# Optimization experiments

Measured on AMD Instinct MI355X. Metric: run time of the kernel, lower is better.

Reference implementation:

```python
import jax, jax.numpy as jnp
import numpy as np

N_NODES = 50000
N_EDGES = 800000
D_IN = 128
D_HID = 128
N_CLASSES = 10


def gcn_conv(x, edge_index, edge_weight, W, b):
    """PyG GCNConv with edge weights: add self-loops, symmetric deg^-1/2 norm,
    gather-scale-scatter aggregation, then bias."""
    n = x.shape[0]
    row, col = edge_index[0], edge_index[1]
    loop = jnp.arange(n)
    row = jnp.concatenate([row, loop])
    col = jnp.concatenate([col, loop])
    ew = jnp.concatenate([edge_weight, jnp.ones((n,), edge_weight.dtype)])
    # degree computed at target nodes (source_to_target flow)
    deg = jax.ops.segment_sum(ew, col, num_segments=n)
    dinv = jnp.where(deg > 0, jax.lax.rsqrt(deg), 0.0)
    norm = dinv[row] * ew * dinv[col]  # [E+N]
    xw = x @ W  # [N, D_HID] dense GEMM first (PyG order)
    msgs = norm[:, None] * xw[row]  # [E+N, D_HID] edge-wise gather+scale
    out = jax.ops.segment_sum(msgs, col, num_segments=n)  # scatter-add
    return out + b


def setup_inputs() -> dict:
    key = jax.random.key(0)
    ks = jax.random.split(key, 9)
    x = jax.random.normal(ks[0], (N_NODES, D_IN), dtype=jnp.float32)
    edge_index = jax.random.randint(ks[1], (2, N_EDGES), 0, N_NODES, dtype=jnp.int64)
    edge_attr = jax.random.uniform(ks[2], (N_EDGES,), dtype=jnp.float32)
    s1 = 1.0 / np.sqrt(D_IN)
    s2 = 1.0 / np.sqrt(D_HID)
    W1 = jax.random.uniform(ks[3], (D_IN, D_HID), minval=-s1, maxval=s1, dtype=jnp.float32)
    b1 = jnp.zeros((D_HID,), jnp.float32)
    W2 = jax.random.uniform(ks[4], (D_HID, D_HID), minval=-s2, maxval=s2, dtype=jnp.float32)
    b2 = jnp.zeros((D_HID,), jnp.float32)
    Wm = jax.random.uniform(ks[5], (D_HID, N_CLASSES), minval=-s2, maxval=s2, dtype=jnp.float32)
    bm = jax.random.uniform(ks[6], (N_CLASSES,), minval=-s2, maxval=s2, dtype=jnp.float32)
    return {"x": x, "edge_index": edge_index, "edge_attr": edge_attr,
            "W1": W1, "b1": b1, "W2": W2, "b2": b2, "Wm": Wm, "bm": bm}


def reference(x, edge_index, edge_attr, W1, b1, W2, b2, Wm, bm):
    h = jax.nn.relu(gcn_conv(x, edge_index, edge_attr, W1, b1))
    h = jax.nn.relu(gcn_conv(h, edge_index, edge_attr, W2, b2))
    # F.dropout(training=False) is identity in eval mode
    g = jnp.mean(h, axis=0)  # [D_HID] graph readout
    return g @ Wm + bm  # [N_CLASSES]
```

## Files before the change

### kernel.cpp

```cpp
#include <hip/hip_runtime.h>

#define DD 128
#define CAP 8192

typedef __attribute__((ext_vector_type(8))) short short8v;
typedef __attribute__((ext_vector_type(4))) float float4v;

__device__ inline unsigned short f2b(float f) {
    unsigned int x = __float_as_uint(f);
    return (unsigned short)((x + 0x7fffu + ((x >> 16) & 1u)) >> 16);
}
__device__ inline float blo(unsigned int u) { return __uint_as_float(u << 16); }
__device__ inline float bhi(unsigned int u) { return __uint_as_float(u & 0xffff0000u); }

__global__ void wconv2_kernel(const float* __restrict__ W1, unsigned short* __restrict__ Wt1h,
                              unsigned short* __restrict__ Wt1l,
                              const float* __restrict__ W2, unsigned short* __restrict__ Wt2h,
                              unsigned short* __restrict__ Wt2l,
                              int* bcnt, int nb) {
    int t = threadIdx.x;
    if (blockIdx.x == 0 && t < nb) bcnt[t] = 0;
    int which = blockIdx.x >> 6;
    int idx = (blockIdx.x & 63) * 256 + t;
    int k = idx >> 7, nn = idx & 127;
    const float* W = which ? W2 : W1;
    unsigned short* Hh = which ? Wt2h : Wt1h;
    unsigned short* Hl = which ? Wt2l : Wt1l;
    float w = W[idx];
    unsigned short hi = f2b(w);
    float rem = w - __uint_as_float(((unsigned int)hi) << 16);
    Hh[nn * 128 + k] = hi;
    Hl[nn * 128 + k] = f2b(rem);
}

__global__ __launch_bounds__(256) void bin_direct_kernel(const int* __restrict__ row,
                                                         const int* __restrict__ col,
                                                         const float* __restrict__ ew,
                                                         int* bcnt, uint2* __restrict__ binned,
                                                         int E) {
    __shared__ int h[256];
    __shared__ int resv[256];
    int t = threadIdx.x;
    h[t] = 0;
    __syncthreads();
    int base = blockIdx.x * 2048;
    int myb[8], myrank[8];
    uint2 myrec[8];
    bool val[8];
#pragma unroll
    for (int j = 0; j < 8; ++j) {
        int e = base + j * 256 + t;
        val[j] = e < E;
        if (val[j]) {
            int c = col[e], r = row[e];
            myb[j] = c >> 8;
            myrank[j] = atomicAdd(&h[myb[j]], 1);
            myrec[j] = make_uint2(__float_as_uint(ew[e]),
                                  ((unsigned int)r << 8) | (unsigned int)(c & 255));
        }
    }
    __syncthreads();
    if (h[t]) resv[t] = atomicAdd(&bcnt[t], h[t]);
    __syncthreads();
#pragma unroll
    for (int j = 0; j < 8; ++j)
        if (val[j]) {
            int pos = resv[myb[j]] + myrank[j];
            if (pos < CAP) binned[(size_t)myb[j] * CAP + pos] = myrec[j];
        }
}

__global__ __launch_bounds__(256) void build_csr_kernel(const uint2* __restrict__ binned,
                                                        const int* __restrict__ bcnt,
                                                        uint2* __restrict__ startend,
                                                        float* __restrict__ dinv,
                                                        unsigned int* __restrict__ sedge, int n) {
    __shared__ unsigned int cnt[256];
    __shared__ unsigned int degf[256];
    __shared__ int sc[256];
    __shared__ int cur[256];
    int b = blockIdx.x, t = threadIdx.x;
    cnt[t] = 0; degf[t] = 0;
    __syncthreads();
    const int total = bcnt[b];
    const uint2* brec = binned + (size_t)b * CAP;
    for (int k = t; k < total; k += 256) {
        uint2 rec = brec[k];
        int cl = rec.y & 255;
        atomicAdd(&cnt[cl], 1u);
        atomicAdd(&degf[cl], (unsigned int)__float2uint_rn(__uint_as_float(rec.x) * 16777216.0f));
    }
    __syncthreads();
    int v = (int)cnt[t];
    sc[t] = v;
    __syncthreads();
    for (int off = 1; off < 256; off <<= 1) {
        int add = t >= off ? sc[t - off] : 0;
        __syncthreads();
        sc[t] += add;
        __syncthreads();
    }
    const int bstart = b * CAP;
    int myStart = bstart + sc[t] - v;
    cur[t] = myStart;
    int node = b * 256 + t;
    if (node < n) {
        startend[node] = make_uint2((unsigned int)myStart, (unsigned int)(myStart + v));
        float deg = 1.0f + (float)((double)degf[t] * (1.0 / 16777216.0));
        dinv[node] = 1.0f / sqrtf(deg);
    }
    __syncthreads();
    for (int k = t; k < total; k += 256) {
        uint2 rec = brec[k];
        int cl = rec.y & 255;
        int r = (int)(rec.y >> 8);
        int pos = atomicAdd(&cur[cl], 1);
        sedge[pos] = ((unsigned int)r << 16) | (unsigned int)f2b(__uint_as_float(rec.x));
    }
}

template <bool F32A>
__global__ __launch_bounds__(256) void mfma_gemm_kernel(const void* __restrict__ Av,
                                                        const unsigned short* __restrict__ WtHi,
                                                        const unsigned short* __restrict__ WtLo,
                                                        const float* __restrict__ dinv,
                                                        unsigned short* __restrict__ C, int n) {
    __shared__ __align__(16) unsigned short WLh[16 * 128 * 8];
    __shared__ __align__(16) unsigned short WLl[16 * 128 * 8];
    const int tid = threadIdx.x;

    for (int c = tid; c < 2048; c += 256) {
        int nn = c >> 4, k8 = c & 15;
        short8v vh = *(const short8v*)(WtHi + nn * 128 + k8 * 8);
        short8v vl = *(const short8v*)(WtLo + nn * 128 + k8 * 8);
        *(short8v*)(WLh + (k8 * 128 + nn) * 8) = vh;
        *(short8v*)(WLl + (k8 * 128 + nn) * 8) = vl;
    }
    __syncthreads();

    const int lane = tid & 63;
    const int l15 = lane & 15, l4 = lane >> 4;
    const int m0 = blockIdx.x * 128 + (tid >> 6) * 32;

    float4v acc[2][8];
#pragma unroll
    for (int i = 0; i < 2; ++i)
#pragma unroll
        for (int j = 0; j < 8; ++j) acc[i][j] = (float4v){0.f, 0.f, 0.f, 0.f};

#pragma unroll
    for (int kb = 0; kb < 4; ++kb) {
        short8v aF[2];
#pragma unroll
        for (int i = 0; i < 2; ++i) {
            int r = m0 + i * 16 + l15;
            r = r < n ? r : n - 1;
            if constexpr (F32A) {
                const float* xr = (const float*)Av + (size_t)r * 128 + kb * 32 + l4 * 8;
                float4 v0 = ((const float4*)xr)[0];
                float4 v1 = ((const float4*)xr)[1];
                short8v a;
                a[0] = (short)f2b(v0.x); a[1] = (short)f2b(v0.y);
                a[2] = (short)f2b(v0.z); a[3] = (short)f2b(v0.w);
                a[4] = (short)f2b(v1.x); a[5] = (short)f2b(v1.y);
                a[6] = (short)f2b(v1.z); a[7] = (short)f2b(v1.w);
                aF[i] = a;
            } else {
                aF[i] = *(const short8v*)((const unsigned short*)Av +
                                          (size_t)r * 128 + kb * 32 + l4 * 8);
            }
        }
        const int k8 = kb * 4 + l4;
#pragma unroll
        for (int j = 0; j < 8; ++j) {
            short8v bh = *(const short8v*)(WLh + (k8 * 128 + j * 16 + l15) * 8);
            short8v bl = *(const short8v*)(WLl + (k8 * 128 + j * 16 + l15) * 8);
            acc[0][j] = __builtin_amdgcn_mfma_f32_16x16x32_bf16(aF[0], bh, acc[0][j], 0, 0, 0);
            acc[1][j] = __builtin_amdgcn_mfma_f32_16x16x32_bf16(aF[1], bh, acc[1][j], 0, 0, 0);
            acc[0][j] = __builtin_amdgcn_mfma_f32_16x16x32_bf16(aF[0], bl, acc[0][j], 0, 0, 0);
            acc[1][j] = __builtin_amdgcn_mfma_f32_16x16x32_bf16(aF[1], bl, acc[1][j], 0, 0, 0);
        }
    }

#pragma unroll
    for (int i = 0; i < 2; ++i)
#pragma unroll
        for (int r = 0; r < 4; ++r) {
            int rr = m0 + i * 16 + l4 * 4 + r;
            if (rr < n) {
                float dvr = dinv[rr];
#pragma unroll
                for (int j = 0; j < 8; ++j)
                    C[(size_t)rr * 128 + j * 16 + l15] = f2b(acc[i][j][r] * dvr);
            }
        }
}

__device__ inline void agg_node(int i, int t, const uint2* __restrict__ startend,
                                const unsigned int* __restrict__ sedge,
                                const float* __restrict__ dinv,
                                const unsigned short* __restrict__ xw,
                                const float* __restrict__ bias,
                                float& a0out, float& a1out) {
    unsigned int u = *(const unsigned int*)(xw + (size_t)i * DD + 2 * t);
    float a0 = blo(u);
    float a1 = bhi(u);
    uint2 se = startend[i];
    int k = (int)se.x;
    const int e = (int)se.y;
    for (; k + 15 < e; k += 16) {
        unsigned int pe[16], uu[16];
        float nv[16];
#pragma unroll
        for (int j = 0; j < 16; ++j) pe[j] = sedge[k + j];
#pragma unroll
        for (int j = 0; j < 16; ++j) {
            nv[j] = __uint_as_float((pe[j] & 0xffffu) << 16);
            uu[j] = *(const unsigned int*)(xw + (size_t)(pe[j] >> 16) * DD + 2 * t);
        }
#pragma unroll
        for (int j = 0; j < 16; ++j) {
            a0 += nv[j] * blo(uu[j]);
            a1 += nv[j] * bhi(uu[j]);
        }
    }
    for (; k + 3 < e; k += 4) {
        unsigned int pe[4], uu[4];
        float nv[4];
#pragma unroll
        for (int j = 0; j < 4; ++j) pe[j] = sedge[k + j];
#pragma unroll
        for (int j = 0; j < 4; ++j) {
            nv[j] = __uint_as_float((pe[j] & 0xffffu) << 16);
            uu[j] = *(const unsigned int*)(xw + (size_t)(pe[j] >> 16) * DD + 2 * t);
        }
#pragma unroll
        for (int j = 0; j < 4; ++j) {
            a0 += nv[j] * blo(uu[j]);
            a1 += nv[j] * bhi(uu[j]);
        }
    }
    for (; k < e; ++k) {
        unsigned int pe = sedge[k];
        float nvv = __uint_as_float((pe & 0xffffu) << 16);
        unsigned int u2 = *(const unsigned int*)(xw + (size_t)(pe >> 16) * DD + 2 * t);
        a0 += nvv * blo(u2);
        a1 += nvv * bhi(u2);
    }
    const float dv = dinv[i];
    a0out = fmaxf(dv * a0 + bias[2 * t], 0.f);
    a1out = fmaxf(dv * a1 + bias[2 * t + 1], 0.f);
}

__global__ __launch_bounds__(256) void agg_kernel(const uint2* __restrict__ startend,
                                                  const unsigned int* __restrict__ sedge,
                                                  const float* __restrict__ dinv,
                                                  const unsigned short* __restrict__ xw,
                                                  const float* __restrict__ bias,
                                                  unsigned short* __restrict__ h, int n) {
    const int i = blockIdx.x * 4 + (threadIdx.x >> 6);
    if (i >= n) return;
    const int t = threadIdx.x & 63;
    float a0, a1;
    agg_node(i, t, startend, sedge, dinv, xw, bias, a0, a1);
    *(unsigned int*)(h + (size_t)i * DD + 2 * t) =
        (unsigned int)f2b(a0) | ((unsigned int)f2b(a1) << 16);
}

__global__ __launch_bounds__(256) void agg_colsum_kernel(const uint2* __restrict__ startend,
                                                         const unsigned int* __restrict__ sedge,
                                                         const float* __restrict__ dinv,
                                                         const unsigned short* __restrict__ xw,
                                                         const float* __restrict__ bias,
                                                         float* __restrict__ partial, int n) {
    __shared__ float red[4][64][2];
    const int w = threadIdx.x >> 6;
    const int t = threadIdx.x & 63;
    const int i = blockIdx.x * 4 + w;
    float a0 = 0.f, a1 = 0.f;
    if (i < n) agg_node(i, t, startend, sedge, dinv, xw, bias, a0, a1);
    red[w][t][0] = a0;
    red[w][t][1] = a1;
    __syncthreads();
    if (threadIdx.x < DD) {
        int f = threadIdx.x, tt = f >> 1, idx = f & 1;
        float s = red[0][tt][idx] + red[1][tt][idx] + red[2][tt][idx] + red[3][tt][idx];
        partial[(size_t)blockIdx.x * DD + f] = s;
    }
}

__global__ __launch_bounds__(128) void colsum2_kernel(const float* __restrict__ partial,
                                                      float* __restrict__ partial2, int nblk) {
    int t = threadIdx.x;
    float acc = 0.f;
    for (int r = blockIdx.x; r < nblk; r += gridDim.x) acc += partial[(size_t)r * DD + t];
    partial2[blockIdx.x * DD + t] = acc;
}

__global__ void final_kernel(const float* __restrict__ partial2, const float* __restrict__ Wm,
                             const float* __restrict__ bm, float* __restrict__ out, int n) {
    __shared__ float g[DD];
    int t = threadIdx.x;
    float acc = 0.f;
    for (int b = 0; b < 512; ++b) acc += partial2[b * DD + t];
    g[t] = acc / (float)n;
    __syncthreads();
    if (t < 10) {
        float o = bm[t];
#pragma unroll
        for (int d = 0; d < DD; ++d) o += g[d] * Wm[d * 10 + t];
        out[t] = o;
    }
}

extern "C" void kernel_launch(void* const* d_in, const int* in_sizes, int n_in,
                              void* d_out, int out_size, void* d_ws, size_t ws_size,
                              hipStream_t stream) {
    const float* x  = (const float*)d_in[0];
    const int*   ei = (const int*)d_in[1];
    const float* ew = (const float*)d_in[2];
    const float* W1 = (const float*)d_in[3];
    const float* b1 = (const float*)d_in[4];
    const float* W2 = (const float*)d_in[5];
    const float* b2 = (const float*)d_in[6];
    const float* Wm = (const float*)d_in[7];
    const float* bm = (const float*)d_in[8];
    float* out = (float*)d_out;

    const int n = in_sizes[0] / DD;
    const int E = in_sizes[2];
    const int* row = ei;
    const int* col = ei + E;

    const int nb = (n + 255) >> 8;
    const int edgeChunks = (E + 2047) / 2048;
    const int aggBlocks = (n + 3) / 4;

    uint2* binned = (uint2*)d_ws;
    unsigned int* sedge = (unsigned int*)(binned + (size_t)nb * CAP);
    float* dinv    = (float*)(sedge + (size_t)nb * CAP);
    uint2* startend = (uint2*)(dinv + n);
    int*   bcnt    = (int*)(startend + n);
    float* partial = (float*)(bcnt + nb);
    float* partial2 = partial + (size_t)aggBlocks * DD;
    uintptr_t p = (uintptr_t)(partial2 + 512 * DD);
    p = (p + 15) & ~(uintptr_t)15;
    unsigned short* T0 = (unsigned short*)p;
    unsigned short* T1 = T0 + (size_t)n * DD;
    unsigned short* Wt1h = T1 + (size_t)n * DD;
    unsigned short* Wt1l = Wt1h + 16384;
    unsigned short* Wt2h = Wt1l + 16384;
    unsigned short* Wt2l = Wt2h + 16384;

    wconv2_kernel<<<128, 256, 0, stream>>>(W1, Wt1h, Wt1l, W2, Wt2h, Wt2l, bcnt, nb);

    bin_direct_kernel<<<edgeChunks, 256, 0, stream>>>(row, col, ew, bcnt, binned, E);
    build_csr_kernel<<<nb, 256, 0, stream>>>(binned, bcnt, startend, dinv, sedge, n);

    const int gemmBlocks = (n + 127) / 128;

    mfma_gemm_kernel<true><<<gemmBlocks, 256, 0, stream>>>(x, Wt1h, Wt1l, dinv, T0, n);
    agg_kernel<<<aggBlocks, 256, 0, stream>>>(startend, sedge, dinv, T0, b1, T1, n);

    mfma_gemm_kernel<false><<<gemmBlocks, 256, 0, stream>>>(T1, Wt2h, Wt2l, dinv, T0, n);
    agg_colsum_kernel<<<aggBlocks, 256, 0, stream>>>(startend, sedge, dinv, T0, b2, partial, n);

    colsum2_kernel<<<512, 128, 0, stream>>>(partial, partial2, aggBlocks);
    final_kernel<<<1, 128, 0, stream>>>(partial2, Wm, bm, out, n);
}
```

Baseline: 168.1 us.

## Split each node's edges across 4 lane groups with 16-byte row gathers

Rewrites the aggregation so each wavefront splits its node's edge list across four 16-lane groups. Each lane loads 16 bytes (8 bf16 features) per neighbor row instead of 4, and the partial sums are combined with cross-lane xor shuffles. The aim is fewer, wider gather instructions and more neighbor rows in flight per wave, which should raise memory-level parallelism for this bandwidth- and latency-bound gather. The cost is extra shuffle reductions, idle predicated lanes on low-degree nodes, and only a quarter of the lanes doing the final store.

```diff
diff --git a/kernel.cpp b/kernel.cpp
--- a/kernel.cpp
+++ b/kernel.cpp
@@ -196,60 +196,63 @@
         }
 }
 
-__device__ inline void agg_node(int i, int t, const uint2* __restrict__ startend,
-                                const unsigned int* __restrict__ sedge,
-                                const float* __restrict__ dinv,
-                                const unsigned short* __restrict__ xw,
-                                const float* __restrict__ bias,
-                                float& a0out, float& a1out) {
-    unsigned int u = *(const unsigned int*)(xw + (size_t)i * DD + 2 * t);
-    float a0 = blo(u);
-    float a1 = bhi(u);
+__device__ inline void agg_node_v4(int i, int sub, int q,
+                                   const uint2* __restrict__ startend,
+                                   const unsigned int* __restrict__ sedge,
+                                   const float* __restrict__ dinv,
+                                   const unsigned short* __restrict__ xw,
+                                   const float* __restrict__ bias,
+                                   float* __restrict__ a) {
+#pragma unroll
+    for (int j = 0; j < 8; ++j) a[j] = 0.f;
+    const uint4* xw4 = (const uint4*)xw;
     uint2 se = startend[i];
-    int k = (int)se.x;
-    const int e = (int)se.y;
-    for (; k + 15 < e; k += 16) {
-        unsigned int pe[16], uu[16];
-        float nv[16];
-#pragma unroll
-        for (int j = 0; j < 16; ++j) pe[j] = sedge[k + j];
-#pragma unroll
-        for (int j = 0; j < 16; ++j) {
-            nv[j] = __uint_as_float((pe[j] & 0xffffu) << 16);
-            uu[j] = *(const unsigned int*)(xw + (size_t)(pe[j] >> 16) * DD + 2 * t);
-        }
-#pragma unroll
-        for (int j = 0; j < 16; ++j) {
-            a0 += nv[j] * blo(uu[j]);
-            a1 += nv[j] * bhi(uu[j]);
-        }
-    }
-    for (; k + 3 < e; k += 4) {
-        unsigned int pe[4], uu[4];
+    const int s = (int)se.x, e = (int)se.y;
+    for (int k = s; k < e; k += 16) {
+        unsigned int pe[4];
+        uint4 u[4];
         float nv[4];
 #pragma unroll
-        for (int j = 0; j < 4; ++j) pe[j] = sedge[k + j];
-#pragma unroll
-        for (int j = 0; j < 4; ++j) {
-            nv[j] = __uint_as_float((pe[j] & 0xffffu) << 16);
-            uu[j] = *(const unsigned int*)(xw + (size_t)(pe[j] >> 16) * DD + 2 * t);
-        }
-#pragma unroll
-        for (int j = 0; j < 4; ++j) {
-            a0 += nv[j] * blo(uu[j]);
-            a1 += nv[j] * bhi(uu[j]);
-        }
-    }
-    for (; k < e; ++k) {
-        unsigned int pe = sedge[k];
-        float nvv = __uint_as_float((pe & 0xffffu) << 16);
-        unsigned int u2 = *(const unsigned int*)(xw + (size_t)(pe >> 16) * DD + 2 * t);
-        a0 += nvv * blo(u2);
-        a1 += nvv * bhi(u2);
+        for (int jj = 0; jj < 4; ++jj) {
+            int idx = k + 4 * jj + sub;
+            bool valid = idx < e;
+            pe[jj] = sedge[valid ? idx : s];
+            nv[jj] = valid ? __uint_as_float((pe[jj] & 0xffffu) << 16) : 0.f;
+        }
+#pragma unroll
+        for (int jj = 0; jj < 4; ++jj)
+            u[jj] = xw4[(size_t)(pe[jj] >> 16) * 16 + q];
+#pragma unroll
+        for (int jj = 0; jj < 4; ++jj) {
+            a[0] += nv[jj] * blo(u[jj].x); a[1] += nv[jj] * bhi(u[jj].x);
+            a[2] += nv[jj] * blo(u[jj].y); a[3] += nv[jj] * bhi(u[jj].y);
+            a[4] += nv[jj] * blo(u[jj].z); a[5] += nv[jj] * bhi(u[jj].z);
+            a[6] += nv[jj] * blo(u[jj].w); a[7] += nv[jj] * bhi(u[jj].w);
+        }
+    }
+    if (sub == 0) {
+        uint4 u = xw4[(size_t)i * 16 + q];
+        a[0] += blo(u.x); a[1] += bhi(u.x);
+        a[2] += blo(u.y); a[3] += bhi(u.y);
+        a[4] += blo(u.z); a[5] += bhi(u.z);
+        a[6] += blo(u.w); a[7] += bhi(u.w);
+    }
+#pragma unroll
+    for (int j = 0; j < 8; ++j) {
+        a[j] += __shfl_xor(a[j], 16);
+        a[j] += __shfl_xor(a[j], 32);
     }
     const float dv = dinv[i];
-    a0out = fmaxf(dv * a0 + bias[2 * t], 0.f);
-    a1out = fmaxf(dv * a1 + bias[2 * t + 1], 0.f);
+    const float4 b0 = ((const float4*)bias)[q * 2];
+    const float4 b1 = ((const float4*)bias)[q * 2 + 1];
+    a[0] = fmaxf(dv * a[0] + b0.x, 0.f);
+    a[1] = fmaxf(dv * a[1] + b0.y, 0.f);
+    a[2] = fmaxf(dv * a[2] + b0.z, 0.f);
+    a[3] = fmaxf(dv * a[3] + b0.w, 0.f);
+    a[4] = fmaxf(dv * a[4] + b1.x, 0.f);
+    a[5] = fmaxf(dv * a[5] + b1.y, 0.f);
+    a[6] = fmaxf(dv * a[6] + b1.z, 0.f);
+    a[7] = fmaxf(dv * a[7] + b1.w, 0.f);
 }
 
 __global__ __launch_bounds__(256) void agg_kernel(const uint2* __restrict__ startend,
@@ -260,11 +263,18 @@
                                                   unsigned short* __restrict__ h, int n) {
     const int i = blockIdx.x * 4 + (threadIdx.x >> 6);
     if (i >= n) return;
-    const int t = threadIdx.x & 63;
-    float a0, a1;
-    agg_node(i, t, startend, sedge, dinv, xw, bias, a0, a1);
-    *(unsigned int*)(h + (size_t)i * DD + 2 * t) =
-        (unsigned int)f2b(a0) | ((unsigned int)f2b(a1) << 16);
+    const int lane = threadIdx.x & 63;
+    const int sub = lane >> 4, q = lane & 15;
+    float a[8];
+    agg_node_v4(i, sub, q, startend, sedge, dinv, xw, bias, a);
+    if (sub == 0) {
+        uint4 o;
+        o.x = (unsigned int)f2b(a[0]) | ((unsigned int)f2b(a[1]) << 16);
+        o.y = (unsigned int)f2b(a[2]) | ((unsigned int)f2b(a[3]) << 16);
+        o.z = (unsigned int)f2b(a[4]) | ((unsigned int)f2b(a[5]) << 16);
+        o.w = (unsigned int)f2b(a[6]) | ((unsigned int)f2b(a[7]) << 16);
+        ((uint4*)h)[(size_t)i * 16 + q] = o;
+    }
 }
 
 __global__ __launch_bounds__(256) void agg_colsum_kernel(const uint2* __restrict__ startend,
@@ -273,18 +283,23 @@
                                                          const unsigned short* __restrict__ xw,
                                                          const float* __restrict__ bias,
                                                          float* __restrict__ partial, int n) {
-    __shared__ float red[4][64][2];
+    __shared__ float red[4][DD];
     const int w = threadIdx.x >> 6;
-    const int t = threadIdx.x & 63;
+    const int lane = threadIdx.x & 63;
+    const int sub = lane >> 4, q = lane & 15;
     const int i = blockIdx.x * 4 + w;
-    float a0 = 0.f, a1 = 0.f;
-    if (i < n) agg_node(i, t, startend, sedge, dinv, xw, bias, a0, a1);
-    red[w][t][0] = a0;
-    red[w][t][1] = a1;
+    float a[8];
+#pragma unroll
+    for (int j = 0; j < 8; ++j) a[j] = 0.f;
+    if (i < n) agg_node_v4(i, sub, q, startend, sedge, dinv, xw, bias, a);
+    if (sub == 0) {
+#pragma unroll
+        for (int j = 0; j < 8; ++j) red[w][q * 8 + j] = a[j];
+    }
     __syncthreads();
     if (threadIdx.x < DD) {
-        int f = threadIdx.x, tt = f >> 1, idx = f & 1;
-        float s = red[0][tt][idx] + red[1][tt][idx] + red[2][tt][idx] + red[3][tt][idx];
+        int f = threadIdx.x;
+        float s = red[0][f] + red[1][f] + red[2][f] + red[3][f];
         partial[(size_t)blockIdx.x * DD + f] = s;
     }
 }
```

New measurement: 163.9 us. 2.6% less time.
